# Kernel optimization log

Measured on AMD Instinct MI355X. Metric: run time of the kernel, lower is better.

Reference implementation:

```python
import jax, jax.numpy as jnp
import numpy as np

B, N, F_DIM, R_DIM = 4, 512, 64, 128


def _pair_indices(n):
    # Same order as the original python double loop: i outer, j inner, skip i==j.
    ii, jj = np.meshgrid(np.arange(n), np.arange(n), indexing='ij')
    mask = ii != jj
    return jnp.asarray(ii[mask]), jnp.asarray(jj[mask])  # each [N*(N-1)]


def setup_inputs() -> dict:
    key = jax.random.key(0)
    ks = jax.random.split(key, 7)
    s1 = 1.0 / np.sqrt(2 * F_DIM)
    s2 = 1.0 / np.sqrt(R_DIM)
    return {
        'features': jax.random.normal(ks[0], (B, N, F_DIM), dtype=jnp.float32),
        'W1': jax.random.uniform(ks[1], (2 * F_DIM, R_DIM), jnp.float32, -s1, s1),
        'b1': jax.random.uniform(ks[2], (R_DIM,), jnp.float32, -s1, s1),
        'W2': jax.random.uniform(ks[3], (R_DIM, R_DIM), jnp.float32, -s2, s2),
        'b2': jax.random.uniform(ks[4], (R_DIM,), jnp.float32, -s2, s2),
        'W3': jax.random.uniform(ks[5], (R_DIM, 1), jnp.float32, -s2, s2),
        'b3': jax.random.uniform(ks[6], (1,), jnp.float32, -s2, s2),
    }


def reference(features, W1, b1, W2, b2, W3, b3):
    n = features.shape[1]
    idx_i, idx_j = _pair_indices(n)
    # Gather all ordered pairs (i != j): [B, P, 2F]
    pair = jnp.concatenate([features[:, idx_i, :], features[:, idx_j, :]], axis=-1)
    h = jax.nn.relu(jnp.einsum('bpf,fr->bpr', pair, W1) + b1)
    h = jax.nn.relu(jnp.einsum('bpr,rs->bps', h, W2) + b2)
    out = jnp.einsum('bpr,ro->bpo', h, W3) + b3  # [B, P, 1]
    return out
```

## Files before the change

### kernel.cpp

```cpp
#include <hip/hip_runtime.h>
#include <stdint.h>

#define B_ 4
#define N_ 512
#define F_ 64
#define R_ 128
#define PPI 511
#define TJ 128

typedef _Float16 f16x8 __attribute__((ext_vector_type(8)));
typedef _Float16 f16x2 __attribute__((ext_vector_type(2)));
typedef float f32x4 __attribute__((ext_vector_type(4)));

__device__ __forceinline__ uint16_t f16bits(float x) {
  return __builtin_bit_cast(uint16_t, (_Float16)x);
}
__device__ __forceinline__ f16x2 cvt_pk(float a, float b) {
  return __builtin_bit_cast(f16x2, __builtin_amdgcn_cvt_pkrtz(a, b));
}

__global__ __launch_bounds__(256) void prep_all(
    const float* __restrict__ feat, const float* __restrict__ W1,
    const float* __restrict__ b1, const float* __restrict__ W2,
    uint16_t* __restrict__ U, uint16_t* __restrict__ V, uint16_t* __restrict__ w2f) {
  if (blockIdx.x >= 512) {
    const int d = (blockIdx.x - 512) * 256 + threadIdx.x;
    const int jj = d & 7, lane = (d >> 3) & 63, tc = d >> 9;
    const int c = tc & 3, t = tc >> 2;
    const int rr = 32 * c + (lane >> 4) * 8 + jj;
    const int s = 16 * t + (lane & 15);
    w2f[d] = f16bits(W2[rr * R_ + s]);
    return;
  }
  __shared__ float fs[4][F_];
  const int row0 = blockIdx.x * 4;
  const int tid = threadIdx.x;
  if (tid < 4 * F_) fs[tid >> 6][tid & 63] = feat[row0 * F_ + tid];
  __syncthreads();
  const int r = tid & 127, rh = tid >> 7;
  float aU[2], aV[2];
  const float bias = b1[r];
#pragma unroll
  for (int ii = 0; ii < 2; ++ii) { aU[ii] = bias; aV[ii] = 0.f; }
#pragma unroll 8
  for (int f = 0; f < F_; ++f) {
    const float wa = W1[f * R_ + r];
    const float wb = W1[(F_ + f) * R_ + r];
#pragma unroll
    for (int ii = 0; ii < 2; ++ii) {
      aU[ii] = fmaf(fs[rh * 2 + ii][f], wa, aU[ii]);
      aV[ii] = fmaf(fs[rh * 2 + ii][f], wb, aV[ii]);
    }
  }
#pragma unroll
  for (int ii = 0; ii < 2; ++ii) {
    const int row = row0 + rh * 2 + ii;
    U[row * R_ + r] = f16bits(aU[ii]);
    V[row * R_ + r] = f16bits(aV[ii]);
  }
}

__global__ __launch_bounds__(256, 3) void relnet_main(
    const uint16_t* __restrict__ U, const uint16_t* __restrict__ V,
    const uint16_t* __restrict__ w2f, const float* __restrict__ b2,
    const float* __restrict__ W3, const float* __restrict__ b3,
    float* __restrict__ out) {
  __shared__ __align__(16) uint16_t Vs[TJ * 128];

  const int bid = blockIdx.x;
  const int jb = bid & 3, ib = (bid >> 2) & 255, b = bid >> 10;
  const int i0 = ib * 2, j0 = jb * TJ;
  const int tid = threadIdx.x;

  {
    const uint4* sv = (const uint4*)(V + (b * N_ + j0) * R_);
    for (int l = tid; l < TJ * 16; l += 256) {
      const int row = l >> 4, seg = l & 15;
      const int col = (seg * 16) ^ ((row & 7) << 4);
      *(uint4*)((char*)Vs + row * 256 + col) = sv[row * 16 + seg];
    }
  }

  const int lane = tid & 63, wave = tid >> 6;
  const int quad = lane >> 4, l4 = lane & 15;
  const int il = wave >> 1, th = wave & 1;
  const int i = i0 + il;

  f16x8 w2r[4][4];
#pragma unroll
  for (int tp = 0; tp < 4; ++tp)
#pragma unroll
    for (int c = 0; c < 4; ++c) {
      const int t = th * 4 + tp;
      const uint4 w = *(const uint4*)(w2f + ((size_t)((t * 4 + c) * 64 + lane)) * 8);
      w2r[tp][c] = __builtin_bit_cast(f16x8, w);
    }

  f32x4 b2f[4];
  f16x2 w3p[4][2];
#pragma unroll
  for (int tp = 0; tp < 4; ++tp) {
    const int s0 = 16 * (th * 4 + tp) + 4 * quad;
    b2f[tp] = (f32x4){b2[s0], b2[s0 + 1], b2[s0 + 2], b2[s0 + 3]};
    w3p[tp][0] = (f16x2){(_Float16)W3[s0], (_Float16)W3[s0 + 1]};
    w3p[tp][1] = (f16x2){(_Float16)W3[s0 + 2], (_Float16)W3[s0 + 3]};
  }

  f16x8 uf[4];
#pragma unroll
  for (int c = 0; c < 4; ++c)
    uf[c] = __builtin_bit_cast(f16x8,
        *(const uint4*)(U + (size_t)(b * N_ + i) * R_ + c * 32 + quad * 8));

  const f16x8 z8 = {};
  const f16x2 z2 = {};

  __syncthreads();

  float res[8];

#pragma unroll
  for (int jt = 0; jt < 8; ++jt) {
    f16x8 hb[4];
#pragma unroll
    for (int c = 0; c < 4; ++c) {
      const uint4 v = *(const uint4*)((const char*)Vs + (jt * 16 + l4) * 256 +
                                      ((c * 64 + quad * 16) ^ ((l4 & 7) << 4)));
      hb[c] = __builtin_elementwise_max(__builtin_bit_cast(f16x8, v) + uf[c], z8);
    }

    f32x4 acc[4];
    __builtin_amdgcn_s_setprio(1);
#pragma unroll
    for (int tp = 0; tp < 4; ++tp)
      acc[tp] = __builtin_amdgcn_mfma_f32_16x16x32_f16(w2r[tp][0], hb[0], b2f[tp], 0, 0, 0);
#pragma unroll
    for (int c = 1; c < 4; ++c)
#pragma unroll
      for (int tp = 0; tp < 4; ++tp)
        acc[tp] = __builtin_amdgcn_mfma_f32_16x16x32_f16(w2r[tp][c], hb[c], acc[tp], 0, 0, 0);
    __builtin_amdgcn_s_setprio(0);

    float t0 = 0.f, t1 = 0.f, t2 = 0.f, t3 = 0.f;
#pragma unroll
    for (int tp = 0; tp < 4; tp += 2) {
      f16x2 p0 = __builtin_elementwise_max(cvt_pk(acc[tp][0], acc[tp][1]), z2);
      f16x2 p1 = __builtin_elementwise_max(cvt_pk(acc[tp][2], acc[tp][3]), z2);
      t0 = __builtin_amdgcn_fdot2(p0, w3p[tp][0], t0, false);
      t1 = __builtin_amdgcn_fdot2(p1, w3p[tp][1], t1, false);
      f16x2 q0 = __builtin_elementwise_max(cvt_pk(acc[tp + 1][0], acc[tp + 1][1]), z2);
      f16x2 q1 = __builtin_elementwise_max(cvt_pk(acc[tp + 1][2], acc[tp + 1][3]), z2);
      t2 = __builtin_amdgcn_fdot2(q0, w3p[tp + 1][0], t2, false);
      t3 = __builtin_amdgcn_fdot2(q1, w3p[tp + 1][1], t3, false);
    }
    res[jt] = (t0 + t1) + (t2 + t3);
  }

  __syncthreads();

  {
    float* pls = (float*)Vs;
    const int base = ((th * 2 + il) * 8) * 64 + quad * 16 + l4;
#pragma unroll
    for (int jt = 0; jt < 8; ++jt) pls[base + jt * 64] = res[jt];
  }

  __syncthreads();

  {
    const float* pls = (const float*)Vs;
    const int ril = tid >> 7, rjt = (tid >> 4) & 7, rl4 = tid & 15;
    float sum = b3[0];
#pragma unroll
    for (int h = 0; h < 2; ++h)
#pragma unroll
      for (int q = 0; q < 4; ++q)
        sum += pls[((h * 2 + ril) * 8 + rjt) * 64 + q * 16 + rl4];
    const int ri = i0 + ril;
    const int j = j0 + rjt * 16 + rl4;
    if (j != ri) {
      const int p = (b * N_ + ri) * PPI + (j < ri ? j : j - 1);
      out[p] = sum;
    }
  }
}

extern "C" void kernel_launch(void* const* d_in, const int* in_sizes, int n_in,
                              void* d_out, int out_size, void* d_ws, size_t ws_size,
                              hipStream_t stream) {
  const float* feat = (const float*)d_in[0];
  const float* W1 = (const float*)d_in[1];
  const float* b1 = (const float*)d_in[2];
  const float* W2 = (const float*)d_in[3];
  const float* b2 = (const float*)d_in[4];
  const float* W3 = (const float*)d_in[5];
  const float* b3 = (const float*)d_in[6];

  uint16_t* U = (uint16_t*)d_ws;
  uint16_t* V = U + (size_t)B_ * N_ * R_;
  uint16_t* w2f = V + (size_t)B_ * N_ * R_;

  prep_all<<<512 + 64, 256, 0, stream>>>(feat, W1, b1, W2, U, V, w2f);
  relnet_main<<<B_ * (N_ / 2) * (N_ / TJ), 256, 0, stream>>>(U, V, w2f, b2, W3, b3,
                                                             (float*)d_out);
}
```

Measured before the change: 103.9 us.

## Split W2 output columns across four waves per row with 512-thread blocks

Doubles the block size to 512 threads so each of the two i-rows is handled by four waves, each computing two of the eight 16-column W2 output tiles instead of four. This halves per-wave MFMA work and W2 register footprint, which should raise occupancy and latency hiding. In exchange, each wave recomputes the relu(U+V) operand from LDS, adding redundant LDS traffic. The final reduction now sums four wave partials per output.

Result: slower. 115.5 us (+11.2%).

```diff
diff --git a/kernel.cpp b/kernel.cpp
--- a/kernel.cpp
+++ b/kernel.cpp
@@ -60,7 +60,7 @@
   }
 }
 
-__global__ __launch_bounds__(256, 3) void relnet_main(
+__global__ __launch_bounds__(512, 4) void relnet_main(
     const uint16_t* __restrict__ U, const uint16_t* __restrict__ V,
     const uint16_t* __restrict__ w2f, const float* __restrict__ b2,
     const float* __restrict__ W3, const float* __restrict__ b3,
@@ -74,7 +74,7 @@
 
   {
     const uint4* sv = (const uint4*)(V + (b * N_ + j0) * R_);
-    for (int l = tid; l < TJ * 16; l += 256) {
+    for (int l = tid; l < TJ * 16; l += 512) {
       const int row = l >> 4, seg = l & 15;
       const int col = (seg * 16) ^ ((row & 7) << 4);
       *(uint4*)((char*)Vs + row * 256 + col) = sv[row * 16 + seg];
@@ -83,24 +83,24 @@
 
   const int lane = tid & 63, wave = tid >> 6;
   const int quad = lane >> 4, l4 = lane & 15;
-  const int il = wave >> 1, th = wave & 1;
+  const int il = wave >> 2, tq = wave & 3;
   const int i = i0 + il;
 
-  f16x8 w2r[4][4];
-#pragma unroll
-  for (int tp = 0; tp < 4; ++tp)
+  f16x8 w2r[2][4];
+#pragma unroll
+  for (int tp = 0; tp < 2; ++tp)
 #pragma unroll
     for (int c = 0; c < 4; ++c) {
-      const int t = th * 4 + tp;
+      const int t = tq * 2 + tp;
       const uint4 w = *(const uint4*)(w2f + ((size_t)((t * 4 + c) * 64 + lane)) * 8);
       w2r[tp][c] = __builtin_bit_cast(f16x8, w);
     }
 
-  f32x4 b2f[4];
-  f16x2 w3p[4][2];
-#pragma unroll
-  for (int tp = 0; tp < 4; ++tp) {
-    const int s0 = 16 * (th * 4 + tp) + 4 * quad;
+  f32x4 b2f[2];
+  f16x2 w3p[2][2];
+#pragma unroll
+  for (int tp = 0; tp < 2; ++tp) {
+    const int s0 = 16 * (tq * 2 + tp) + 4 * quad;
     b2f[tp] = (f32x4){b2[s0], b2[s0 + 1], b2[s0 + 2], b2[s0 + 3]};
     w3p[tp][0] = (f16x2){(_Float16)W3[s0], (_Float16)W3[s0 + 1]};
     w3p[tp][1] = (f16x2){(_Float16)W3[s0 + 2], (_Float16)W3[s0 + 3]};
@@ -129,29 +129,28 @@
       hb[c] = __builtin_elementwise_max(__builtin_bit_cast(f16x8, v) + uf[c], z8);
     }
 
-    f32x4 acc[4];
+    f32x4 acc[2];
     __builtin_amdgcn_s_setprio(1);
 #pragma unroll
-    for (int tp = 0; tp < 4; ++tp)
+    for (int tp = 0; tp < 2; ++tp)
       acc[tp] = __builtin_amdgcn_mfma_f32_16x16x32_f16(w2r[tp][0], hb[0], b2f[tp], 0, 0, 0);
 #pragma unroll
     for (int c = 1; c < 4; ++c)
 #pragma unroll
-      for (int tp = 0; tp < 4; ++tp)
+      for (int tp = 0; tp < 2; ++tp)
         acc[tp] = __builtin_amdgcn_mfma_f32_16x16x32_f16(w2r[tp][c], hb[c], acc[tp], 0, 0, 0);
     __builtin_amdgcn_s_setprio(0);
 
     float t0 = 0.f, t1 = 0.f, t2 = 0.f, t3 = 0.f;
-#pragma unroll
-    for (int tp = 0; tp < 4; tp += 2) {
-      f16x2 p0 = __builtin_elementwise_max(cvt_pk(acc[tp][0], acc[tp][1]), z2);
-      f16x2 p1 = __builtin_elementwise_max(cvt_pk(acc[tp][2], acc[tp][3]), z2);
-      t0 = __builtin_amdgcn_fdot2(p0, w3p[tp][0], t0, false);
-      t1 = __builtin_amdgcn_fdot2(p1, w3p[tp][1], t1, false);
-      f16x2 q0 = __builtin_elementwise_max(cvt_pk(acc[tp + 1][0], acc[tp + 1][1]), z2);
-      f16x2 q1 = __builtin_elementwise_max(cvt_pk(acc[tp + 1][2], acc[tp + 1][3]), z2);
-      t2 = __builtin_amdgcn_fdot2(q0, w3p[tp + 1][0], t2, false);
-      t3 = __builtin_amdgcn_fdot2(q1, w3p[tp + 1][1], t3, false);
+    {
+      const f16x2 p0 = __builtin_elementwise_max(cvt_pk(acc[0][0], acc[0][1]), z2);
+      const f16x2 p1 = __builtin_elementwise_max(cvt_pk(acc[0][2], acc[0][3]), z2);
+      t0 = __builtin_amdgcn_fdot2(p0, w3p[0][0], t0, false);
+      t1 = __builtin_amdgcn_fdot2(p1, w3p[0][1], t1, false);
+      const f16x2 q0 = __builtin_elementwise_max(cvt_pk(acc[1][0], acc[1][1]), z2);
+      const f16x2 q1 = __builtin_elementwise_max(cvt_pk(acc[1][2], acc[1][3]), z2);
+      t2 = __builtin_amdgcn_fdot2(q0, w3p[1][0], t2, false);
+      t3 = __builtin_amdgcn_fdot2(q1, w3p[1][1], t3, false);
     }
     res[jt] = (t0 + t1) + (t2 + t3);
   }
@@ -160,26 +159,27 @@
 
   {
     float* pls = (float*)Vs;
-    const int base = ((th * 2 + il) * 8) * 64 + quad * 16 + l4;
+    const int base = wave * 512 + quad * 16 + l4;
 #pragma unroll
     for (int jt = 0; jt < 8; ++jt) pls[base + jt * 64] = res[jt];
   }
 
   __syncthreads();
 
-  {
+  if (tid < 2 * TJ) {
     const float* pls = (const float*)Vs;
-    const int ril = tid >> 7, rjt = (tid >> 4) & 7, rl4 = tid & 15;
+    const int ril = tid >> 7, j = tid & 127;
+    const int rjt = j >> 4, rl4 = j & 15;
     float sum = b3[0];
 #pragma unroll
-    for (int h = 0; h < 2; ++h)
+    for (int tq2 = 0; tq2 < 4; ++tq2)
 #pragma unroll
       for (int q = 0; q < 4; ++q)
-        sum += pls[((h * 2 + ril) * 8 + rjt) * 64 + q * 16 + rl4];
+        sum += pls[(ril * 4 + tq2) * 512 + rjt * 64 + q * 16 + rl4];
     const int ri = i0 + ril;
-    const int j = j0 + rjt * 16 + rl4;
-    if (j != ri) {
-      const int p = (b * N_ + ri) * PPI + (j < ri ? j : j - 1);
+    const int jg = j0 + j;
+    if (jg != ri) {
+      const int p = (b * N_ + ri) * PPI + (jg < ri ? jg : jg - 1);
       out[p] = sum;
     }
   }
@@ -201,6 +201,6 @@
   uint16_t* w2f = V + (size_t)B_ * N_ * R_;
 
   prep_all<<<512 + 64, 256, 0, stream>>>(feat, W1, b1, W2, U, V, w2f);
-  relnet_main<<<B_ * (N_ / 2) * (N_ / TJ), 256, 0, stream>>>(U, V, w2f, b2, W3, b3,
+  relnet_main<<<B_ * (N_ / 2) * (N_ / TJ), 512, 0, stream>>>(U, V, w2f, b2, W3, b3,
                                                              (float*)d_out);
 }
```

## Restructure prep kernel to stage W1 in LDS and compute 16 rows per thread

Applied to the files above, without the earlier changes.

The prep kernel now handles 32 feature rows per block instead of 4. It copies all of W1 (64KB) into shared memory, stores the feature tile transposed, and gives each thread 16 rows of U and V outputs so each W1 load is reused across many FMAs. This cuts global W1 traffic and the block count from 576 to 128, but it uses a large LDS footprint and has far fewer blocks, so occupancy and parallelism drop.

Measured after the change: 109.2 us. 5.1% more time.

```diff
diff --git a/kernel.cpp b/kernel.cpp
--- a/kernel.cpp
+++ b/kernel.cpp
@@ -23,8 +23,8 @@
     const float* __restrict__ feat, const float* __restrict__ W1,
     const float* __restrict__ b1, const float* __restrict__ W2,
     uint16_t* __restrict__ U, uint16_t* __restrict__ V, uint16_t* __restrict__ w2f) {
-  if (blockIdx.x >= 512) {
-    const int d = (blockIdx.x - 512) * 256 + threadIdx.x;
+  if (blockIdx.x >= 64) {
+    const int d = (blockIdx.x - 64) * 256 + threadIdx.x;
     const int jj = d & 7, lane = (d >> 3) & 63, tc = d >> 9;
     const int c = tc & 3, t = tc >> 2;
     const int rr = 32 * c + (lane >> 4) * 8 + jj;
@@ -32,31 +32,66 @@
     w2f[d] = f16bits(W2[rr * R_ + s]);
     return;
   }
-  __shared__ float fs[4][F_];
-  const int row0 = blockIdx.x * 4;
+  __shared__ __align__(16) float W1s[2 * F_ * R_];
+  __shared__ __align__(16) float fT[F_ * 36];
+
   const int tid = threadIdx.x;
-  if (tid < 4 * F_) fs[tid >> 6][tid & 63] = feat[row0 * F_ + tid];
-  __syncthreads();
+  const int row0 = blockIdx.x * 32;
+
+  {
+    const uint4* s = (const uint4*)W1;
+    uint4* d = (uint4*)W1s;
+#pragma unroll
+    for (int k = 0; k < 16; ++k) d[tid + 256 * k] = s[tid + 256 * k];
+  }
+  {
+    const float4* fs = (const float4*)(feat + (size_t)row0 * F_);
+    const float4 a = fs[tid * 2];
+    const float4 b = fs[tid * 2 + 1];
+    const int row = tid >> 3, f0 = (tid & 7) * 8;
+    fT[(f0 + 0) * 36 + row] = a.x;
+    fT[(f0 + 1) * 36 + row] = a.y;
+    fT[(f0 + 2) * 36 + row] = a.z;
+    fT[(f0 + 3) * 36 + row] = a.w;
+    fT[(f0 + 4) * 36 + row] = b.x;
+    fT[(f0 + 5) * 36 + row] = b.y;
+    fT[(f0 + 6) * 36 + row] = b.z;
+    fT[(f0 + 7) * 36 + row] = b.w;
+  }
+  __syncthreads();
+
   const int r = tid & 127, rh = tid >> 7;
-  float aU[2], aV[2];
+  float u[16], v[16];
   const float bias = b1[r];
 #pragma unroll
-  for (int ii = 0; ii < 2; ++ii) { aU[ii] = bias; aV[ii] = 0.f; }
-#pragma unroll 8
+  for (int j = 0; j < 16; ++j) { u[j] = bias; v[j] = 0.f; }
+
+#pragma unroll 4
   for (int f = 0; f < F_; ++f) {
-    const float wa = W1[f * R_ + r];
-    const float wb = W1[(F_ + f) * R_ + r];
-#pragma unroll
-    for (int ii = 0; ii < 2; ++ii) {
-      aU[ii] = fmaf(fs[rh * 2 + ii][f], wa, aU[ii]);
-      aV[ii] = fmaf(fs[rh * 2 + ii][f], wb, aV[ii]);
-    }
-  }
-#pragma unroll
-  for (int ii = 0; ii < 2; ++ii) {
-    const int row = row0 + rh * 2 + ii;
-    U[row * R_ + r] = f16bits(aU[ii]);
-    V[row * R_ + r] = f16bits(aV[ii]);
+    const float wa = W1s[f * R_ + r];
+    const float wb = W1s[(F_ + f) * R_ + r];
+    const f32x4 x0 = *(const f32x4*)&fT[f * 36 + rh * 16 + 0];
+    const f32x4 x1 = *(const f32x4*)&fT[f * 36 + rh * 16 + 4];
+    const f32x4 x2 = *(const f32x4*)&fT[f * 36 + rh * 16 + 8];
+    const f32x4 x3 = *(const f32x4*)&fT[f * 36 + rh * 16 + 12];
+#pragma unroll
+    for (int k = 0; k < 4; ++k) {
+      u[0 + k] = fmaf(x0[k], wa, u[0 + k]);
+      v[0 + k] = fmaf(x0[k], wb, v[0 + k]);
+      u[4 + k] = fmaf(x1[k], wa, u[4 + k]);
+      v[4 + k] = fmaf(x1[k], wb, v[4 + k]);
+      u[8 + k] = fmaf(x2[k], wa, u[8 + k]);
+      v[8 + k] = fmaf(x2[k], wb, v[8 + k]);
+      u[12 + k] = fmaf(x3[k], wa, u[12 + k]);
+      v[12 + k] = fmaf(x3[k], wb, v[12 + k]);
+    }
+  }
+
+#pragma unroll
+  for (int j = 0; j < 16; ++j) {
+    const int row = row0 + rh * 16 + j;
+    U[(size_t)row * R_ + r] = f16bits(u[j]);
+    V[(size_t)row * R_ + r] = f16bits(v[j]);
   }
 }
 
@@ -200,7 +235,7 @@
   uint16_t* V = U + (size_t)B_ * N_ * R_;
   uint16_t* w2f = V + (size_t)B_ * N_ * R_;
 
-  prep_all<<<512 + 64, 256, 0, stream>>>(feat, W1, b1, W2, U, V, w2f);
+  prep_all<<<64 + 64, 256, 0, stream>>>(feat, W1, b1, W2, U, V, w2f);
   relnet_main<<<B_ * (N_ / 2) * (N_ / TJ), 256, 0, stream>>>(U, V, w2f, b2, W3, b3,
                                                              (float*)d_out);
 }
```
